# Kernel optimization log

Hardware: AMD Instinct MI355X
Metric: run time of the kernel (lower is better)

Reference implementation:

```python
import jax, jax.numpy as jnp
import numpy as np

D_MODEL = 1024
D_STATE = 16
DT_RANK = 64
BATCH = 4
SEQ = 4096


def setup_inputs() -> dict:
    key = jax.random.key(0)
    ks = jax.random.split(key, 6)
    x = jax.random.normal(ks[0], (BATCH, SEQ, D_MODEL), dtype=jnp.float32)
    # torch nn.Linear weights: (out_features, in_features)
    W_xproj = jax.random.normal(ks[1], (DT_RANK + 2 * D_STATE, D_MODEL), dtype=jnp.float32) * (1.0 / np.sqrt(D_MODEL))
    W_dt = jax.random.normal(ks[2], (D_MODEL, DT_RANK), dtype=jnp.float32) * (1.0 / np.sqrt(DT_RANK))
    b_dt = jax.random.normal(ks[3], (D_MODEL,), dtype=jnp.float32) * 0.01
    A_log = jax.random.normal(ks[4], (D_MODEL, D_STATE), dtype=jnp.float32)
    D = jax.random.normal(ks[5], (D_MODEL,), dtype=jnp.float32)
    return {"x": x, "W_xproj": W_xproj, "W_dt": W_dt, "b_dt": b_dt, "A_log": A_log, "D": D}


def _selective_scan(x, delta, A, B, C):
    # x, delta: (b, s, d); B, C: (b, s, n); A: (d, n)
    b, s, d = x.shape
    n = A.shape[1]
    h0 = jnp.zeros((b, d, n), dtype=x.dtype)

    def step(h, inp):
        x_t, dt_t, B_t, C_t = inp  # (b,d), (b,d), (b,n), (b,n)
        dA = jnp.exp(dt_t[:, :, None] * A[None, :, :])        # (b,d,n)
        dB = dt_t[:, :, None] * B_t[:, None, :]               # (b,d,n)
        h = h * dA + x_t[:, :, None] * dB                     # (b,d,n)
        y_t = jnp.einsum('bdn,bn->bd', h, C_t)                # (b,d)
        return h, y_t

    # time-major for scan
    xs = (jnp.swapaxes(x, 0, 1), jnp.swapaxes(delta, 0, 1),
          jnp.swapaxes(B, 0, 1), jnp.swapaxes(C, 0, 1))
    _, ys = jax.lax.scan(step, h0, xs)  # ys: (s, b, d)
    return jnp.swapaxes(ys, 0, 1)


def reference(x, W_xproj, W_dt, b_dt, A_log, D):
    xp = jnp.einsum('bsd,pd->bsp', x, W_xproj)                # (b,s,dt_rank+2n)
    delta = jax.nn.softplus(jnp.einsum('bsr,dr->bsd', xp[..., :DT_RANK], W_dt) + b_dt)
    B = xp[..., DT_RANK:DT_RANK + D_STATE]
    C = xp[..., DT_RANK + D_STATE:]
    A = -jnp.exp(A_log)
    y = _selective_scan(x, delta, A, B, C)
    return y + x * D[None, None, :]
```

## Files before the change

### kernel.cpp

```cpp
#include <hip/hip_runtime.h>
#include <cstddef>

#define D_MODEL 1024
#define D_STATE 16
#define DT_RANK 64
#define BATCH 4
#define SEQ 4096
#define NPROJ 96
#define M_TOTAL (BATCH * SEQ)
#define NCHUNK 64
#define CLEN 64
#define KSPLIT 4
#define KSLICE 256

typedef __attribute__((ext_vector_type(8))) short bf16x8;
typedef __attribute__((ext_vector_type(4))) short short4v;
typedef __attribute__((ext_vector_type(4))) float f32x4;

__device__ __forceinline__ float softplus_fast(float v) {
    return fmaxf(v, 0.0f) + __logf(1.0f + __expf(-fabsf(v)));
}

__device__ __forceinline__ short f2bf(float x) {
    union { float f; unsigned u; } v; v.f = x;
    unsigned r = (v.u + 0x7fffu + ((v.u >> 16) & 1u)) >> 16;
    return (short)r;
}
__device__ __forceinline__ float bf2f(short s) {
    union { unsigned u; float f; } v; v.u = ((unsigned)(unsigned short)s) << 16;
    return v.f;
}
struct bfpair { short hi, lo; };
__device__ __forceinline__ bfpair split_bf(float x) {
    bfpair r;
    r.hi = f2bf(x);
    r.lo = f2bf(x - bf2f(r.hi));
    return r;
}
__device__ __forceinline__ void split_bf4(float4 v, short4v& h, short4v& l) {
    bfpair a = split_bf(v.x), b = split_bf(v.y), c = split_bf(v.z), d = split_bf(v.w);
    h = (short4v){a.hi, b.hi, c.hi, d.hi};
    l = (short4v){a.lo, b.lo, c.lo, d.lo};
}

__global__ __launch_bounds__(256) void proj_mfma_kernel(const float* __restrict__ x,
                                                        const float* __restrict__ W,
                                                        float* __restrict__ part) {
    __shared__ short ah[64][40], al[64][40];
    __shared__ short bh[96][40], bl[96][40];
    const int tid   = threadIdx.x;
    const int row0  = blockIdx.x * 64;
    const int kbase = blockIdx.y * KSLICE;
    const int wid   = tid >> 6;
    const int lane  = tid & 63;
    const int l16   = lane & 15;
    const int kg    = lane >> 4;

    f32x4 acc[6];
#pragma unroll
    for (int c = 0; c < 6; ++c) acc[c] = (f32x4){0.f, 0.f, 0.f, 0.f};

    for (int k0 = kbase; k0 < kbase + KSLICE; k0 += 32) {
        for (int i = tid; i < 64 * 8; i += 256) {
            int r = i >> 3, c4 = i & 7;
            float4 v = *reinterpret_cast<const float4*>(
                &x[(size_t)(row0 + r) * 1024 + k0 + c4 * 4]);
            short4v h, l;
            split_bf4(v, h, l);
            *reinterpret_cast<short4v*>(&ah[r][c4 * 4]) = h;
            *reinterpret_cast<short4v*>(&al[r][c4 * 4]) = l;
        }
        for (int i = tid; i < 96 * 8; i += 256) {
            int r = i >> 3, c4 = i & 7;
            float4 v = *reinterpret_cast<const float4*>(
                &W[(size_t)r * 1024 + k0 + c4 * 4]);
            short4v h, l;
            split_bf4(v, h, l);
            *reinterpret_cast<short4v*>(&bh[r][c4 * 4]) = h;
            *reinterpret_cast<short4v*>(&bl[r][c4 * 4]) = l;
        }
        __syncthreads();

        bf16x8 a_h = *reinterpret_cast<const bf16x8*>(&ah[wid * 16 + l16][kg * 8]);
        bf16x8 a_l = *reinterpret_cast<const bf16x8*>(&al[wid * 16 + l16][kg * 8]);
#pragma unroll
        for (int c = 0; c < 6; ++c) {
            bf16x8 b_h = *reinterpret_cast<const bf16x8*>(&bh[c * 16 + l16][kg * 8]);
            bf16x8 b_l = *reinterpret_cast<const bf16x8*>(&bl[c * 16 + l16][kg * 8]);
            acc[c] = __builtin_amdgcn_mfma_f32_16x16x32_bf16(a_h, b_h, acc[c], 0, 0, 0);
            acc[c] = __builtin_amdgcn_mfma_f32_16x16x32_bf16(a_h, b_l, acc[c], 0, 0, 0);
            acc[c] = __builtin_amdgcn_mfma_f32_16x16x32_bf16(a_l, b_h, acc[c], 0, 0, 0);
        }
        __syncthreads();
    }
    size_t base = ((size_t)blockIdx.y * M_TOTAL + row0 + wid * 16 + kg * 4) * NPROJ;
#pragma unroll
    for (int c = 0; c < 6; ++c) {
#pragma unroll
        for (int q = 0; q < 4; ++q)
            part[base + (size_t)q * NPROJ + c * 16 + l16] = acc[c][q];
    }
}

__global__ __launch_bounds__(256) void reduce_xp_kernel(const float* __restrict__ part,
                                                        float* __restrict__ xp) {
    const size_t stride4 = (size_t)M_TOTAL * NPROJ / 4;
    size_t i = (size_t)blockIdx.x * 256 + threadIdx.x;
    const float4* p = reinterpret_cast<const float4*>(part);
    float4 a = p[i];
#pragma unroll
    for (int s = 1; s < KSPLIT; ++s) {
        float4 b = p[i + (size_t)s * stride4];
        a.x += b.x; a.y += b.y; a.z += b.z; a.w += b.w;
    }
    reinterpret_cast<float4*>(xp)[i] = a;
}

__global__ __launch_bounds__(256) void delta_mfma_kernel(const float* __restrict__ xp,
                                                         const float* __restrict__ Wd,
                                                         const float* __restrict__ b_dt,
                                                         float* __restrict__ delta) {
    __shared__ short ah[64][72], al[64][72];
    __shared__ short bh[64][72], bl[64][72];
    const int tid  = threadIdx.x;
    const int row0 = blockIdx.x * 64;
    const int col0 = blockIdx.y * 64;
    const int wid  = tid >> 6;
    const int lane = tid & 63;
    const int l16  = lane & 15;
    const int kg   = lane >> 4;

    for (int i = tid; i < 64 * 16; i += 256) {
        int r = i >> 4, c4 = i & 15;
        float4 v = *reinterpret_cast<const float4*>(
            &xp[(size_t)(row0 + r) * NPROJ + c4 * 4]);
        short4v h, l;
        split_bf4(v, h, l);
        *reinterpret_cast<short4v*>(&ah[r][c4 * 4]) = h;
        *reinterpret_cast<short4v*>(&al[r][c4 * 4]) = l;
    }
    for (int i = tid; i < 64 * 16; i += 256) {
        int r = i >> 4, c4 = i & 15;
        float4 v = *reinterpret_cast<const float4*>(
            &Wd[(size_t)(col0 + r) * 64 + c4 * 4]);
        short4v h, l;
        split_bf4(v, h, l);
        *reinterpret_cast<short4v*>(&bh[r][c4 * 4]) = h;
        *reinterpret_cast<short4v*>(&bl[r][c4 * 4]) = l;
    }
    __syncthreads();

    f32x4 acc[4];
#pragma unroll
    for (int j = 0; j < 4; ++j) acc[j] = (f32x4){0.f, 0.f, 0.f, 0.f};

#pragma unroll
    for (int ks = 0; ks < 2; ++ks) {
        int koff = ks * 32 + kg * 8;
        bf16x8 a_h = *reinterpret_cast<const bf16x8*>(&ah[wid * 16 + l16][koff]);
        bf16x8 a_l = *reinterpret_cast<const bf16x8*>(&al[wid * 16 + l16][koff]);
#pragma unroll
        for (int j = 0; j < 4; ++j) {
            bf16x8 b_h = *reinterpret_cast<const bf16x8*>(&bh[j * 16 + l16][koff]);
            bf16x8 b_l = *reinterpret_cast<const bf16x8*>(&bl[j * 16 + l16][koff]);
            acc[j] = __builtin_amdgcn_mfma_f32_16x16x32_bf16(a_h, b_h, acc[j], 0, 0, 0);
            acc[j] = __builtin_amdgcn_mfma_f32_16x16x32_bf16(a_h, b_l, acc[j], 0, 0, 0);
            acc[j] = __builtin_amdgcn_mfma_f32_16x16x32_bf16(a_l, b_h, acc[j], 0, 0, 0);
        }
    }

    int row = row0 + wid * 16 + kg * 4;
#pragma unroll
    for (int j = 0; j < 4; ++j) {
        int col = col0 + j * 16 + l16;
        float bias = b_dt[col];
#pragma unroll
        for (int q = 0; q < 4; ++q)
            delta[(size_t)(row + q) * D_MODEL + col] = softplus_fast(acc[j][q] + bias);
    }
}

__global__ __launch_bounds__(256) void scanA_kernel(const float* __restrict__ x,
                                                    const float* __restrict__ xp,
                                                    const float* __restrict__ delta,
                                                    const float* __restrict__ A_log,
                                                    float* __restrict__ P,
                                                    float* __restrict__ H) {
    const int chunk = blockIdx.x;
    const int b     = blockIdx.z;
    const int d     = blockIdx.y * 256 + threadIdx.x;
    const float LOG2E = 1.4426950408889634f;

    float Av[16];
    const float4* Arow = reinterpret_cast<const float4*>(A_log + (size_t)d * D_STATE);
#pragma unroll
    for (int q = 0; q < 4; ++q) {
        float4 v = Arow[q];
        Av[q*4+0] = -__expf(v.x) * LOG2E; Av[q*4+1] = -__expf(v.y) * LOG2E;
        Av[q*4+2] = -__expf(v.z) * LOG2E; Av[q*4+3] = -__expf(v.w) * LOG2E;
    }
    float h[16];
#pragma unroll
    for (int n = 0; n < 16; ++n) h[n] = 0.0f;
    float sdv = 0.0f;

    const size_t m0 = (size_t)b * SEQ + (size_t)chunk * CLEN;
    const size_t xbase = m0 * D_MODEL + d;
    const size_t pbase = m0 * NPROJ + DT_RANK;

#pragma unroll 2
    for (int j = 0; j < CLEN; ++j) {
        float dv = delta[xbase + (size_t)j * D_MODEL];
        float xv = x[xbase + (size_t)j * D_MODEL];
        float dtx = dv * xv;
        const float4* Bp = reinterpret_cast<const float4*>(xp + pbase + (size_t)j * NPROJ);
        float4 B0 = Bp[0], B1 = Bp[1], B2 = Bp[2], B3 = Bp[3];
        float Bv[16] = {B0.x,B0.y,B0.z,B0.w, B1.x,B1.y,B1.z,B1.w,
                        B2.x,B2.y,B2.z,B2.w, B3.x,B3.y,B3.z,B3.w};
        sdv += dv;
#pragma unroll
        for (int n = 0; n < 16; ++n) {
            float a = exp2f(dv * Av[n]);
            h[n] = fmaf(a, h[n], dtx * Bv[n]);
        }
    }
    size_t idx = (((size_t)chunk * BATCH + b) * D_MODEL + d) * D_STATE;
    float4* Pp = reinterpret_cast<float4*>(P + idx);
    float4* Hp = reinterpret_cast<float4*>(H + idx);
#pragma unroll
    for (int q = 0; q < 4; ++q) {
        float4 pv, hv;
        pv.x = exp2f(Av[q*4+0] * sdv); pv.y = exp2f(Av[q*4+1] * sdv);
        pv.z = exp2f(Av[q*4+2] * sdv); pv.w = exp2f(Av[q*4+3] * sdv);
        hv.x = h[q*4+0]; hv.y = h[q*4+1]; hv.z = h[q*4+2]; hv.w = h[q*4+3];
        Pp[q] = pv; Hp[q] = hv;
    }
}

__global__ __launch_bounds__(256) void scanB_kernel(float* __restrict__ P,
                                                    const float* __restrict__ H) {
    const int t = blockIdx.x * 256 + threadIdx.x;
    float carry = 0.0f;
    for (int c = 0; c < NCHUNK; ++c) {
        size_t idx = (size_t)c * (BATCH * D_MODEL * D_STATE) + t;
        float p  = P[idx];
        float hh = H[idx];
        P[idx] = carry;
        carry = fmaf(p, carry, hh);
    }
}

__global__ __launch_bounds__(256) void scanC_kernel(const float* __restrict__ x,
                                                    const float* __restrict__ xp,
                                                    const float* __restrict__ delta,
                                                    const float* __restrict__ A_log,
                                                    const float* __restrict__ Dvec,
                                                    const float* __restrict__ Hin,
                                                    float* __restrict__ out) {
    const int chunk = blockIdx.x;
    const int b     = blockIdx.z;
    const int d     = blockIdx.y * 256 + threadIdx.x;
    const float LOG2E = 1.4426950408889634f;

    float Av[16];
    const float4* Arow = reinterpret_cast<const float4*>(A_log + (size_t)d * D_STATE);
#pragma unroll
    for (int q = 0; q < 4; ++q) {
        float4 v = Arow[q];
        Av[q*4+0] = -__expf(v.x) * LOG2E; Av[q*4+1] = -__expf(v.y) * LOG2E;
        Av[q*4+2] = -__expf(v.z) * LOG2E; Av[q*4+3] = -__expf(v.w) * LOG2E;
    }
    const float Dv = Dvec[d];

    float h[16];
    size_t idx = (((size_t)chunk * BATCH + b) * D_MODEL + d) * D_STATE;
    const float4* Hp = reinterpret_cast<const float4*>(Hin + idx);
#pragma unroll
    for (int q = 0; q < 4; ++q) {
        float4 v = Hp[q];
        h[q*4+0] = v.x; h[q*4+1] = v.y; h[q*4+2] = v.z; h[q*4+3] = v.w;
    }

    const size_t m0 = (size_t)b * SEQ + (size_t)chunk * CLEN;
    const size_t xbase = m0 * D_MODEL + d;
    const size_t pbase = m0 * NPROJ + DT_RANK;

#pragma unroll 2
    for (int j = 0; j < CLEN; ++j) {
        float dv = delta[xbase + (size_t)j * D_MODEL];
        float xv = x[xbase + (size_t)j * D_MODEL];
        float dtx = dv * xv;
        const float4* Bp = reinterpret_cast<const float4*>(xp + pbase + (size_t)j * NPROJ);
        float4 B0 = Bp[0], B1 = Bp[1], B2 = Bp[2], B3 = Bp[3];
        float4 C0 = Bp[4], C1 = Bp[5], C2 = Bp[6], C3 = Bp[7];
        float Bv[16] = {B0.x,B0.y,B0.z,B0.w, B1.x,B1.y,B1.z,B1.w,
                        B2.x,B2.y,B2.z,B2.w, B3.x,B3.y,B3.z,B3.w};
        float Cv[16] = {C0.x,C0.y,C0.z,C0.w, C1.x,C1.y,C1.z,C1.w,
                        C2.x,C2.y,C2.z,C2.w, C3.x,C3.y,C3.z,C3.w};
        float y = 0.0f;
#pragma unroll
        for (int n = 0; n < 16; ++n) {
            float a = exp2f(dv * Av[n]);
            h[n] = fmaf(a, h[n], dtx * Bv[n]);
            y = fmaf(h[n], Cv[n], y);
        }
        out[xbase + (size_t)j * D_MODEL] = fmaf(xv, Dv, y);
    }
}

extern "C" void kernel_launch(void* const* d_in, const int* in_sizes, int n_in,
                              void* d_out, int out_size, void* d_ws, size_t ws_size,
                              hipStream_t stream) {
    const float* x    = (const float*)d_in[0];
    const float* Wx   = (const float*)d_in[1];
    const float* Wd   = (const float*)d_in[2];
    const float* bdt  = (const float*)d_in[3];
    const float* Alog = (const float*)d_in[4];
    const float* Dv   = (const float*)d_in[5];
    float* out = (float*)d_out;

    float* ws    = (float*)d_ws;
    float* xp    = ws;
    float* delta = xp + (size_t)M_TOTAL * NPROJ;
    float* scan0 = delta + (size_t)M_TOTAL * D_MODEL;
    float* part  = scan0;
    float* P     = scan0;
    float* H     = scan0 + (size_t)NCHUNK * BATCH * D_MODEL * D_STATE;

    proj_mfma_kernel<<<dim3(M_TOTAL / 64, KSPLIT), 256, 0, stream>>>(x, Wx, part);
    reduce_xp_kernel<<<dim3((M_TOTAL * NPROJ / 4) / 256), 256, 0, stream>>>(part, xp);
    delta_mfma_kernel<<<dim3(M_TOTAL / 64, D_MODEL / 64), 256, 0, stream>>>(xp, Wd, bdt, delta);
    scanA_kernel<<<dim3(NCHUNK, 4, BATCH), 256, 0, stream>>>(x, xp, delta, Alog, P, H);
    scanB_kernel<<<dim3((BATCH * D_MODEL * D_STATE) / 256), 256, 0, stream>>>(P, H);
    scanC_kernel<<<dim3(NCHUNK, 4, BATCH), 256, 0, stream>>>(x, xp, delta, Alog, Dv, P, out);
}
```

Baseline: 347.4 us.

## Halve scan chunk length and stage B/C rows in shared memory

The chunk length drops from 64 to 32 timesteps, doubling the number of chunks so the scanA/scanC grids expose more parallelism. Each block now loads its chunk's B (and C) projections into LDS once, instead of every thread reading them from global memory on each step. The C-dot accumulation is split into four partial sums to shorten the dependency chain. In exchange, the sequential scanB pass over chunks gets twice as long, the P/H buffers double in size, and each block pays an extra barrier.

Result: no change. 351.4 us (+1.2%).

```diff
diff --git a/kernel.cpp b/kernel.cpp
--- a/kernel.cpp
+++ b/kernel.cpp
@@ -8,8 +8,8 @@
 #define SEQ 4096
 #define NPROJ 96
 #define M_TOTAL (BATCH * SEQ)
-#define NCHUNK 64
-#define CLEN 64
+#define NCHUNK 128
+#define CLEN 32
 #define KSPLIT 4
 #define KSLICE 256
 
@@ -186,10 +186,20 @@
                                                     const float* __restrict__ A_log,
                                                     float* __restrict__ P,
                                                     float* __restrict__ H) {
+    __shared__ float Bs[CLEN][16];
     const int chunk = blockIdx.x;
     const int b     = blockIdx.z;
-    const int d     = blockIdx.y * 256 + threadIdx.x;
+    const int tid   = threadIdx.x;
+    const int d     = blockIdx.y * 256 + tid;
     const float LOG2E = 1.4426950408889634f;
+
+    const size_t m0 = (size_t)b * SEQ + (size_t)chunk * CLEN;
+    if (tid < CLEN * 4) {
+        int j = tid >> 2, q = tid & 3;
+        float4 v = *reinterpret_cast<const float4*>(
+            xp + (m0 + j) * NPROJ + DT_RANK + q * 4);
+        *reinterpret_cast<float4*>(&Bs[j][q * 4]) = v;
+    }
 
     float Av[16];
     const float4* Arow = reinterpret_cast<const float4*>(A_log + (size_t)d * D_STATE);
@@ -204,24 +214,22 @@
     for (int n = 0; n < 16; ++n) h[n] = 0.0f;
     float sdv = 0.0f;
 
-    const size_t m0 = (size_t)b * SEQ + (size_t)chunk * CLEN;
     const size_t xbase = m0 * D_MODEL + d;
-    const size_t pbase = m0 * NPROJ + DT_RANK;
-
-#pragma unroll 2
+    __syncthreads();
+
+#pragma unroll 4
     for (int j = 0; j < CLEN; ++j) {
         float dv = delta[xbase + (size_t)j * D_MODEL];
         float xv = x[xbase + (size_t)j * D_MODEL];
         float dtx = dv * xv;
-        const float4* Bp = reinterpret_cast<const float4*>(xp + pbase + (size_t)j * NPROJ);
-        float4 B0 = Bp[0], B1 = Bp[1], B2 = Bp[2], B3 = Bp[3];
-        float Bv[16] = {B0.x,B0.y,B0.z,B0.w, B1.x,B1.y,B1.z,B1.w,
-                        B2.x,B2.y,B2.z,B2.w, B3.x,B3.y,B3.z,B3.w};
         sdv += dv;
 #pragma unroll
-        for (int n = 0; n < 16; ++n) {
-            float a = exp2f(dv * Av[n]);
-            h[n] = fmaf(a, h[n], dtx * Bv[n]);
+        for (int g = 0; g < 4; ++g) {
+            float4 Bq = *reinterpret_cast<const float4*>(&Bs[j][g * 4]);
+            h[g*4+0] = fmaf(exp2f(dv * Av[g*4+0]), h[g*4+0], dtx * Bq.x);
+            h[g*4+1] = fmaf(exp2f(dv * Av[g*4+1]), h[g*4+1], dtx * Bq.y);
+            h[g*4+2] = fmaf(exp2f(dv * Av[g*4+2]), h[g*4+2], dtx * Bq.z);
+            h[g*4+3] = fmaf(exp2f(dv * Av[g*4+3]), h[g*4+3], dtx * Bq.w);
         }
     }
     size_t idx = (((size_t)chunk * BATCH + b) * D_MODEL + d) * D_STATE;
@@ -257,10 +265,20 @@
                                                     const float* __restrict__ Dvec,
                                                     const float* __restrict__ Hin,
                                                     float* __restrict__ out) {
+    __shared__ float BCs[CLEN][32];
     const int chunk = blockIdx.x;
     const int b     = blockIdx.z;
-    const int d     = blockIdx.y * 256 + threadIdx.x;
+    const int tid   = threadIdx.x;
+    const int d     = blockIdx.y * 256 + tid;
     const float LOG2E = 1.4426950408889634f;
+
+    const size_t m0 = (size_t)b * SEQ + (size_t)chunk * CLEN;
+    {
+        int j = tid >> 3, q = tid & 7;
+        float4 v = *reinterpret_cast<const float4*>(
+            xp + (m0 + j) * NPROJ + DT_RANK + q * 4);
+        *reinterpret_cast<float4*>(&BCs[j][q * 4]) = v;
+    }
 
     float Av[16];
     const float4* Arow = reinterpret_cast<const float4*>(A_log + (size_t)d * D_STATE);
@@ -281,29 +299,30 @@
         h[q*4+0] = v.x; h[q*4+1] = v.y; h[q*4+2] = v.z; h[q*4+3] = v.w;
     }
 
-    const size_t m0 = (size_t)b * SEQ + (size_t)chunk * CLEN;
     const size_t xbase = m0 * D_MODEL + d;
-    const size_t pbase = m0 * NPROJ + DT_RANK;
-
-#pragma unroll 2
+    __syncthreads();
+
+#pragma unroll 4
     for (int j = 0; j < CLEN; ++j) {
         float dv = delta[xbase + (size_t)j * D_MODEL];
         float xv = x[xbase + (size_t)j * D_MODEL];
         float dtx = dv * xv;
-        const float4* Bp = reinterpret_cast<const float4*>(xp + pbase + (size_t)j * NPROJ);
-        float4 B0 = Bp[0], B1 = Bp[1], B2 = Bp[2], B3 = Bp[3];
-        float4 C0 = Bp[4], C1 = Bp[5], C2 = Bp[6], C3 = Bp[7];
-        float Bv[16] = {B0.x,B0.y,B0.z,B0.w, B1.x,B1.y,B1.z,B1.w,
-                        B2.x,B2.y,B2.z,B2.w, B3.x,B3.y,B3.z,B3.w};
-        float Cv[16] = {C0.x,C0.y,C0.z,C0.w, C1.x,C1.y,C1.z,C1.w,
-                        C2.x,C2.y,C2.z,C2.w, C3.x,C3.y,C3.z,C3.w};
-        float y = 0.0f;
-#pragma unroll
-        for (int n = 0; n < 16; ++n) {
-            float a = exp2f(dv * Av[n]);
-            h[n] = fmaf(a, h[n], dtx * Bv[n]);
-            y = fmaf(h[n], Cv[n], y);
-        }
+        float y0 = 0.f, y1 = 0.f, y2 = 0.f, y3 = 0.f;
+#pragma unroll
+        for (int g = 0; g < 4; ++g) {
+            float4 Bq = *reinterpret_cast<const float4*>(&BCs[j][g * 4]);
+            float4 Cq = *reinterpret_cast<const float4*>(&BCs[j][16 + g * 4]);
+            float h0 = fmaf(exp2f(dv * Av[g*4+0]), h[g*4+0], dtx * Bq.x);
+            float h1 = fmaf(exp2f(dv * Av[g*4+1]), h[g*4+1], dtx * Bq.y);
+            float h2 = fmaf(exp2f(dv * Av[g*4+2]), h[g*4+2], dtx * Bq.z);
+            float h3 = fmaf(exp2f(dv * Av[g*4+3]), h[g*4+3], dtx * Bq.w);
+            h[g*4+0] = h0; h[g*4+1] = h1; h[g*4+2] = h2; h[g*4+3] = h3;
+            y0 = fmaf(h0, Cq.x, y0);
+            y1 = fmaf(h1, Cq.y, y1);
+            y2 = fmaf(h2, Cq.z, y2);
+            y3 = fmaf(h3, Cq.w, y3);
+        }
+        float y = (y0 + y1) + (y2 + y3);
         out[xbase + (size_t)j * D_MODEL] = fmaf(xv, Dv, y);
     }
 }
```
